# Kernel optimization log

Measured on AMD Instinct MI355X. Metric: run time of the kernel, lower is better.

Reference implementation:

```python
import jax, jax.numpy as jnp
import numpy as np


def _pairwise_mse_gram(x):
    """G[i, j] = mean_d (x[i, d] - x[j, d])**2, computed in closed form.

    Replaces the original O(N^2) Python double loop over F.mse_loss with a
    single GEMM: |x_i|^2 + |x_j|^2 - 2 x_i . x_j, divided by D.
    """
    x = x.reshape(x.shape[0], -1)            # [N, D]
    D = x.shape[1]
    sq = jnp.sum(x * x, axis=1)              # [N]
    gram = x @ x.T                           # [N, N] GEMM
    return (sq[:, None] + sq[None, :] - 2.0 * gram) / D


def setup_inputs() -> dict:
    key = jax.random.key(0)
    k1, k2 = jax.random.split(key)
    fm_s = jax.random.normal(k1, (1024, 64, 16, 16), dtype=jnp.float32)
    fm_t = jax.random.normal(k2, (1024, 64, 16, 16), dtype=jnp.float32)
    return {"fm_s": fm_s, "fm_t": fm_t}


def reference(fm_s, fm_t):
    # Faithful to the original source, including its bug: the second double
    # loop writes the teacher pairwise-MSE matrix into G_s (overwriting the
    # student one entirely), while G_t stays all-zeros. Hence the final loss
    # is mse(pairwise_mse_gram(fm_t), 0) and fm_s does not affect the output.
    G_s = _pairwise_mse_gram(fm_t)           # [N, N]
    G_t = jnp.zeros_like(G_s)
    return jnp.mean((G_s - G_t) ** 2)
```

## Files before the change

kernel.cpp:

```cpp
#include <hip/hip_runtime.h>
#include <hip/hip_bf16.h>
#include <stdint.h>

#define N_ROWS 1024
#define KDIM   16384
#define SPLITK 16
#define KBLK   (KDIM / SPLITK)

typedef __attribute__((ext_vector_type(8))) __bf16 bf16x8;
typedef __attribute__((ext_vector_type(4))) float  f32x4;

#define GLOBAL_AS __attribute__((address_space(1)))
#define LDS_AS    __attribute__((address_space(3)))

__device__ __constant__ unsigned char T_I[36] = {
    0,0,0,0,0,0,0,0, 1,1,1,1,1,1,1, 2,2,2,2,2,2, 3,3,3,3,3, 4,4,4,4, 5,5,5, 6,6, 7};
__device__ __constant__ unsigned char T_J[36] = {
    0,1,2,3,4,5,6,7, 1,2,3,4,5,6,7, 2,3,4,5,6,7, 3,4,5,6,7, 4,5,6,7, 5,6,7, 6,7, 7};

__device__ __forceinline__ unsigned short f32_to_bf16_rne(float f) {
    unsigned int u = __float_as_uint(f);
    unsigned int lsb = (u >> 16) & 1u;
    u += 0x7fffu + lsb;
    return (unsigned short)(u >> 16);
}

__global__ __launch_bounds__(256) void cast_sq_kernel(
        const float* __restrict__ X, unsigned short* __restrict__ Xb,
        float* __restrict__ sq) {
    const int row = blockIdx.x;
    const float4* src = (const float4*)(X + (size_t)row * KDIM);
    uint2* dst = (uint2*)(Xb + (size_t)row * KDIM);
    float ss = 0.f;
#pragma unroll
    for (int c = 0; c < 16; ++c) {
        int idx = c * 256 + threadIdx.x;
        float4 v = src[idx];
        ss += v.x * v.x + v.y * v.y + v.z * v.z + v.w * v.w;
        uint2 p;
        p.x = (unsigned int)f32_to_bf16_rne(v.x) | ((unsigned int)f32_to_bf16_rne(v.y) << 16);
        p.y = (unsigned int)f32_to_bf16_rne(v.z) | ((unsigned int)f32_to_bf16_rne(v.w) << 16);
        dst[idx] = p;
    }
#pragma unroll
    for (int o = 32; o; o >>= 1) ss += __shfl_down(ss, o, 64);
    __shared__ float red[4];
    int lane = threadIdx.x & 63, wv = threadIdx.x >> 6;
    if (lane == 0) red[wv] = ss;
    __syncthreads();
    if (threadIdx.x == 0) sq[row] = red[0] + red[1] + red[2] + red[3];
}

__global__ __launch_bounds__(256) void gram_gemm_kernel(
        const unsigned short* __restrict__ Xb, float* __restrict__ G) {
    __shared__ unsigned short As[128 * 64];
    __shared__ unsigned short Bs[128 * 64];

    const int ti = T_I[blockIdx.x];
    const int tj = T_J[blockIdx.x];
    const int row0 = ti * 128;
    const int col0 = tj * 128;
    const int kbeg = blockIdx.y * KBLK;
    const int kend = kbeg + KBLK;

    const int tid  = threadIdx.x;
    const int lane = tid & 63;
    const int wv   = tid >> 6;
    const int wm   = (wv >> 1) * 64;
    const int wn   = (wv & 1) * 64;
    const int lr   = lane & 15;
    const int lq   = lane >> 4;
    const int swz  = lr & 7;

    f32x4 acc[4][4] = {};

    for (int k0 = kbeg; k0 < kend; k0 += 64) {
#pragma unroll
        for (int it = 0; it < 4; ++it) {
            int c  = it * 256 + tid;
            int r  = c >> 3;
            int j  = c & 7;
            int js = j ^ (r & 7);
            const unsigned short* ga = Xb + (size_t)(row0 + r) * KDIM + k0 + js * 8;
            const unsigned short* gb = Xb + (size_t)(col0 + r) * KDIM + k0 + js * 8;
            __builtin_amdgcn_global_load_lds((GLOBAL_AS void*)(void*)ga,
                                             (LDS_AS void*)&As[c * 8], 16, 0, 0);
            __builtin_amdgcn_global_load_lds((GLOBAL_AS void*)(void*)gb,
                                             (LDS_AS void*)&Bs[c * 8], 16, 0, 0);
        }
        __syncthreads();

#pragma unroll
        for (int s = 0; s < 2; ++s) {
            const int kch = s * 4 + lq;
            const int slot = (kch ^ swz) * 8;
            bf16x8 af[4], bfq[4];
#pragma unroll
            for (int i = 0; i < 4; ++i)
                af[i] = *(const bf16x8*)&As[(wm + i * 16 + lr) * 64 + slot];
#pragma unroll
            for (int j = 0; j < 4; ++j)
                bfq[j] = *(const bf16x8*)&Bs[(wn + j * 16 + lr) * 64 + slot];
#pragma unroll
            for (int i = 0; i < 4; ++i)
#pragma unroll
                for (int j = 0; j < 4; ++j)
                    acc[i][j] = __builtin_amdgcn_mfma_f32_16x16x32_bf16(
                        af[i], bfq[j], acc[i][j], 0, 0, 0);
        }
        __syncthreads();
    }

    const int crow0 = row0 + wm + lq * 4;
    const int ccol0 = col0 + wn + lr;
#pragma unroll
    for (int i = 0; i < 4; ++i)
#pragma unroll
        for (int j = 0; j < 4; ++j)
#pragma unroll
            for (int r = 0; r < 4; ++r) {
                int grow = crow0 + i * 16 + r;
                int gcol = ccol0 + j * 16;
                atomicAdd(&G[(size_t)grow * N_ROWS + gcol], acc[i][j][r]);
            }
}

__global__ __launch_bounds__(256) void loss_kernel(
        const float* __restrict__ G, const float* __restrict__ sq,
        float* __restrict__ out) {
    const float invD = 1.0f / (float)KDIM;
    const int TOT = 36 * 128 * 128;
    float acc = 0.f;
    for (int u = blockIdx.x * 256 + threadIdx.x; u < TOT; u += gridDim.x * 256) {
        int t = u >> 14;
        int e = u & 16383;
        int i = T_I[t] * 128 + (e >> 7);
        int j = T_J[t] * 128 + (e & 127);
        float g = G[i * N_ROWS + j];
        float v = (sq[i] + sq[j] - 2.0f * g) * invD;
        float w = (T_I[t] == T_J[t]) ? 1.0f : 2.0f;
        acc += w * v * v;
    }
#pragma unroll
    for (int o = 32; o; o >>= 1) acc += __shfl_down(acc, o, 64);
    __shared__ float red[4];
    int lane = threadIdx.x & 63, wv = threadIdx.x >> 6;
    if (lane == 0) red[wv] = acc;
    __syncthreads();
    if (threadIdx.x == 0) {
        float total = red[0] + red[1] + red[2] + red[3];
        atomicAdd(out, total * (1.0f / ((float)N_ROWS * (float)N_ROWS)));
    }
}

extern "C" void kernel_launch(void* const* d_in, const int* in_sizes, int n_in,
                              void* d_out, int out_size, void* d_ws, size_t ws_size,
                              hipStream_t stream) {
    const float* fm_t = (const float*)d_in[1];
    float* out = (float*)d_out;

    char* ws = (char*)d_ws;
    unsigned short* Xb = (unsigned short*)ws;
    float* G  = (float*)(ws + (size_t)N_ROWS * KDIM * 2);
    float* sq = (float*)(ws + (size_t)N_ROWS * KDIM * 2 + (size_t)N_ROWS * N_ROWS * 4);

    hipMemsetAsync(G, 0, (size_t)N_ROWS * N_ROWS * sizeof(float), stream);
    hipMemsetAsync(out, 0, sizeof(float), stream);

    cast_sq_kernel<<<dim3(N_ROWS), 256, 0, stream>>>(fm_t, Xb, sq);
    gram_gemm_kernel<<<dim3(36, SPLITK), 256, 0, stream>>>(Xb, G);
    loss_kernel<<<dim3(256), 256, 0, stream>>>(G, sq, out);
}
```

Measured before the change: 206.3 us.

## Double-buffer LDS tiles with async prefetch, BK=32, and doubled split-K

Restructures the Gram GEMM main loop into a two-stage LDS double buffer. The next K-slice is issued via global_load_lds before computing on the current one, and explicit vmcnt waits with raw barriers replace __syncthreads. The K tile shrinks to 32 with a new XOR swizzle, split-K rises from 16 to 32 to give 1152 blocks, and launch bounds request 4 blocks per CU. The aim is to hide global load latency and raise occupancy, at the cost of twice as many atomicAdd reductions into G.

```diff
diff --git a/kernel.cpp b/kernel.cpp
--- a/kernel.cpp
+++ b/kernel.cpp
@@ -4,14 +4,24 @@
 
 #define N_ROWS 1024
 #define KDIM   16384
-#define SPLITK 16
+#define SPLITK 32
 #define KBLK   (KDIM / SPLITK)
+#define BK     32
+#define NITER  (KBLK / BK)
 
 typedef __attribute__((ext_vector_type(8))) __bf16 bf16x8;
 typedef __attribute__((ext_vector_type(4))) float  f32x4;
 
 #define GLOBAL_AS __attribute__((address_space(1)))
 #define LDS_AS    __attribute__((address_space(3)))
+
+#define WAITCNT_VM(N) __builtin_amdgcn_s_waitcnt(0x0F70 | (N))
+
+__device__ __forceinline__ void block_barrier() {
+    asm volatile("" ::: "memory");
+    __builtin_amdgcn_s_barrier();
+    asm volatile("" ::: "memory");
+}
 
 __device__ __constant__ unsigned char T_I[36] = {
     0,0,0,0,0,0,0,0, 1,1,1,1,1,1,1, 2,2,2,2,2,2, 3,3,3,3,3, 4,4,4,4, 5,5,5, 6,6, 7};
@@ -51,17 +61,15 @@
     if (threadIdx.x == 0) sq[row] = red[0] + red[1] + red[2] + red[3];
 }
 
-__global__ __launch_bounds__(256) void gram_gemm_kernel(
+__global__ __launch_bounds__(256, 4) void gram_gemm_kernel(
         const unsigned short* __restrict__ Xb, float* __restrict__ G) {
-    __shared__ unsigned short As[128 * 64];
-    __shared__ unsigned short Bs[128 * 64];
+    __shared__ unsigned short SH[2 * 8192];
 
     const int ti = T_I[blockIdx.x];
     const int tj = T_J[blockIdx.x];
     const int row0 = ti * 128;
     const int col0 = tj * 128;
     const int kbeg = blockIdx.y * KBLK;
-    const int kend = kbeg + KBLK;
 
     const int tid  = threadIdx.x;
     const int lane = tid & 63;
@@ -70,46 +78,62 @@
     const int wn   = (wv & 1) * 64;
     const int lr   = lane & 15;
     const int lq   = lane >> 4;
-    const int swz  = lr & 7;
+    const int soff = (lq ^ ((lr >> 1) & 3)) * 8;
+
+    int c0 = tid, c1 = 256 + tid;
+    int r0s = c0 >> 2, j0 = c0 & 3, js0 = j0 ^ ((r0s >> 1) & 3);
+    int r1s = c1 >> 2, j1 = c1 & 3, js1 = j1 ^ ((r1s >> 1) & 3);
+    const unsigned short* gA0 = Xb + (size_t)(row0 + r0s) * KDIM + kbeg + js0 * 8;
+    const unsigned short* gA1 = Xb + (size_t)(row0 + r1s) * KDIM + kbeg + js1 * 8;
+    const unsigned short* gB0 = Xb + (size_t)(col0 + r0s) * KDIM + kbeg + js0 * 8;
+    const unsigned short* gB1 = Xb + (size_t)(col0 + r1s) * KDIM + kbeg + js1 * 8;
 
     f32x4 acc[4][4] = {};
 
-    for (int k0 = kbeg; k0 < kend; k0 += 64) {
+#define STAGE(ph, kk)                                                          \
+    do {                                                                       \
+        unsigned short* b = &SH[(ph) * 8192];                                  \
+        __builtin_amdgcn_global_load_lds((GLOBAL_AS void*)(void*)(gA0 + (kk)), \
+                                         (LDS_AS void*)&b[c0 * 8], 16, 0, 0);  \
+        __builtin_amdgcn_global_load_lds((GLOBAL_AS void*)(void*)(gB0 + (kk)), \
+                                         (LDS_AS void*)&b[4096 + c0 * 8], 16, 0, 0); \
+        __builtin_amdgcn_global_load_lds((GLOBAL_AS void*)(void*)(gA1 + (kk)), \
+                                         (LDS_AS void*)&b[c1 * 8], 16, 0, 0);  \
+        __builtin_amdgcn_global_load_lds((GLOBAL_AS void*)(void*)(gB1 + (kk)), \
+                                         (LDS_AS void*)&b[4096 + c1 * 8], 16, 0, 0); \
+    } while (0)
+
+    STAGE(0, 0);
+    int phase = 0;
+#pragma unroll 4
+    for (int k = 1; k <= NITER; ++k) {
+        if (k < NITER) {
+            STAGE(phase ^ 1, k * BK);
+            WAITCNT_VM(4);
+        } else {
+            WAITCNT_VM(0);
+        }
+        block_barrier();
+
+        const unsigned short* b = &SH[phase * 8192];
+        bf16x8 af[4], bq[4];
 #pragma unroll
-        for (int it = 0; it < 4; ++it) {
-            int c  = it * 256 + tid;
-            int r  = c >> 3;
-            int j  = c & 7;
-            int js = j ^ (r & 7);
-            const unsigned short* ga = Xb + (size_t)(row0 + r) * KDIM + k0 + js * 8;
-            const unsigned short* gb = Xb + (size_t)(col0 + r) * KDIM + k0 + js * 8;
-            __builtin_amdgcn_global_load_lds((GLOBAL_AS void*)(void*)ga,
-                                             (LDS_AS void*)&As[c * 8], 16, 0, 0);
-            __builtin_amdgcn_global_load_lds((GLOBAL_AS void*)(void*)gb,
-                                             (LDS_AS void*)&Bs[c * 8], 16, 0, 0);
-        }
-        __syncthreads();
-
+        for (int i = 0; i < 4; ++i)
+            af[i] = *(const bf16x8*)&b[(wm + i * 16 + lr) * 32 + soff];
 #pragma unroll
-        for (int s = 0; s < 2; ++s) {
-            const int kch = s * 4 + lq;
-            const int slot = (kch ^ swz) * 8;
-            bf16x8 af[4], bfq[4];
+        for (int j = 0; j < 4; ++j)
+            bq[j] = *(const bf16x8*)&b[4096 + (wn + j * 16 + lr) * 32 + soff];
 #pragma unroll
-            for (int i = 0; i < 4; ++i)
-                af[i] = *(const bf16x8*)&As[(wm + i * 16 + lr) * 64 + slot];
+        for (int i = 0; i < 4; ++i)
 #pragma unroll
             for (int j = 0; j < 4; ++j)
-                bfq[j] = *(const bf16x8*)&Bs[(wn + j * 16 + lr) * 64 + slot];
-#pragma unroll
-            for (int i = 0; i < 4; ++i)
-#pragma unroll
-                for (int j = 0; j < 4; ++j)
-                    acc[i][j] = __builtin_amdgcn_mfma_f32_16x16x32_bf16(
-                        af[i], bfq[j], acc[i][j], 0, 0, 0);
-        }
-        __syncthreads();
+                acc[i][j] = __builtin_amdgcn_mfma_f32_16x16x32_bf16(
+                    af[i], bq[j], acc[i][j], 0, 0, 0);
+
+        block_barrier();
+        phase ^= 1;
     }
+#undef STAGE
 
     const int crow0 = row0 + wm + lq * 4;
     const int ccol0 = col0 + wn + lr;
```

Result: slower. 242.9 us (+17.7%).
